# Kernel optimization log

Hardware: AMD Instinct MI355X
Metric: run time of the kernel (lower is better)

The kernel has to match this reference:

```python
import jax, jax.numpy as jnp
import numpy as np
from jax.scipy.special import gammaln

MAP_W, MAP_H, T_SIZE = 64, 64, 64  # map_sizes
NUM_CP = 8
BATCH = 128


def setup_inputs() -> dict:
    key = jax.random.key(0)
    k1, k2, k3 = jax.random.split(key, 3)
    # control-point means on the pixel grid [0, 63]
    cp_means = jax.random.uniform(k1, (NUM_CP, BATCH, 2), dtype=jnp.float32) * 63.0
    # PSD, well-conditioned 2x2 covariances: A A^T * 2 + 4 I
    A = jax.random.normal(k2, (NUM_CP, BATCH, 2, 2), dtype=jnp.float32)
    cp_covariances = jnp.einsum('kbij,kbpj->kbip', A, A) * 2.0 + 4.0 * jnp.eye(2, dtype=jnp.float32)
    # each curve uses between 3 and NUM_CP control points
    num_cps = jax.random.randint(k3, (BATCH,), 3, NUM_CP + 1, dtype=jnp.int64 if jax.config.jax_enable_x64 else jnp.int32)
    return {"cp_means": cp_means, "num_cps": num_cps, "cp_covariances": cp_covariances}


def _bezier_weights(num_cps, num_cp, t):
    # binomial_coefs[i, b] = binom(num_cps[b]-1, i) for i < num_cps[b], else 0
    k = jnp.arange(num_cp, dtype=jnp.float32)[:, None]          # (K,1)
    n = (num_cps - 1).astype(jnp.float32)[None, :]              # (1,B)
    valid = k <= n
    nk = jnp.where(valid, n - k, 0.0)
    coef = jnp.where(valid, jnp.exp(gammaln(n + 1.0) - gammaln(k + 1.0) - gammaln(nk + 1.0)), 0.0)  # (K,B)
    pot = jnp.maximum(n - k, 0.0)                               # pot[pot<0]=0
    # Bernstein basis weights: (K, B, T)
    w = coef[:, :, None] * (t[None, None, :] ** k[:, :, None]) * ((1.0 - t)[None, None, :] ** pot[:, :, None])
    return w


def reference(cp_means, num_cps, cp_covariances):
    num_cp = cp_means.shape[0]
    t = jnp.linspace(0.0, 1.0, T_SIZE, dtype=jnp.float32)
    w = _bezier_weights(num_cps, num_cp, t)                      # (K,B,T)
    mean = jnp.einsum('kbt,kbd->btd', w, cp_means)               # (B,T,2)
    cov = jnp.einsum('kbt,kbij->btij', w * w, cp_covariances)    # (B,T,2,2)

    # pixel grid positions: pos[x, y] = (x, y)
    xs = jnp.arange(MAP_W, dtype=jnp.float32)
    ys = jnp.arange(MAP_H, dtype=jnp.float32)
    pos = jnp.stack(jnp.meshgrid(xs, ys, indexing='ij'), axis=-1)  # (W,H,2)

    d = pos[None, :, :, None, :] - mean[:, None, None, :, :]      # (B,W,H,T,2)

    # closed-form 2x2 inverse and determinant
    a, b = cov[..., 0, 0], cov[..., 0, 1]
    c, dd = cov[..., 1, 0], cov[..., 1, 1]
    det = a * dd - b * c                                          # (B,T)
    inv = jnp.stack([jnp.stack([dd, -b], -1), jnp.stack([-c, a], -1)], -2) / det[..., None, None]

    q = jnp.einsum('bxyti,btij,bxytj->bxyt', d, inv, d)           # (B,W,H,T)
    divisor = jnp.sqrt((2.0 * np.pi) ** 2 * det)                  # (B,T)
    return jnp.exp(-0.5 * q) / divisor[:, None, None, :]
```

## Files before the change

### kernel.cpp

```cpp
#include <hip/hip_runtime.h>
#include <hip/hip_bf16.h>


#define MAP_W 64
#define MAP_H 64
#define T_SIZE 64
#define NUM_CP 8
#define BATCH 128

__global__ __launch_bounds__(256) void pmap_kernel(
    const void* __restrict__ cp_means_p,
    const void* __restrict__ num_cps_p,
    const void* __restrict__ cp_cov_p,
    float* __restrict__ out)
{
    __shared__ float s_my[T_SIZE], s_g11[T_SIZE], s_c0[T_SIZE], s_c1[T_SIZE], s_sc[T_SIZE];

    const int tid = threadIdx.x;
    const int blk = blockIdx.x;
    const int b   = blk >> 6;
    const int x   = blk & 63;

    if (tid < T_SIZE) {
        const int* ni32 = (const int*)num_cps_p;
        const bool is_i64 = (ni32[1] == 0);
        const int  ncp = is_i64 ? (int)((const long long*)num_cps_p)[b] : ni32[b];
        const int  n   = ncp - 1;

        const __hip_bfloat16* mbv = (const __hip_bfloat16*)cp_means_p;
        const __hip_bfloat16* cbv = (const __hip_bfloat16*)cp_cov_p;
        const float*          mf  = (const float*)cp_means_p;
        const float*          cf  = (const float*)cp_cov_p;
        bool is_f32 = false;
        #pragma unroll
        for (int i = 0; i < 32; ++i) {
            const float v = __bfloat162float(mbv[i]);
            if (!(v >= 0.0f && v <= 64.0f)) is_f32 = true;
        }

        const float t   = (float)tid * (1.0f / 63.0f);
        const float omt = 1.0f - t;

        float mx = 0.f, my = 0.f, ca = 0.f, cb = 0.f, cc = 0.f, cd = 0.f;
        float ck = 1.0f, tk = 1.0f;
        #pragma unroll
        for (int k = 0; k < NUM_CP; ++k) {
            const int e = n - k;
            float onk = (e == 0) ? 1.0f : 0.0f;
            float o = 1.0f;
            #pragma unroll
            for (int j = 1; j < NUM_CP; ++j) { o *= omt; if (e == j) onk = o; }
            const float w  = (k <= n) ? ck * tk * onk : 0.0f;
            const float w2 = w * w;
            const int base = k * BATCH + b;
            const float m0 = is_f32 ? mf[base*2+0] : __bfloat162float(mbv[base*2+0]);
            const float m1 = is_f32 ? mf[base*2+1] : __bfloat162float(mbv[base*2+1]);
            const float q0 = is_f32 ? cf[base*4+0] : __bfloat162float(cbv[base*4+0]);
            const float q1 = is_f32 ? cf[base*4+1] : __bfloat162float(cbv[base*4+1]);
            const float q2 = is_f32 ? cf[base*4+2] : __bfloat162float(cbv[base*4+2]);
            const float q3 = is_f32 ? cf[base*4+3] : __bfloat162float(cbv[base*4+3]);
            mx = fmaf(w,  m0, mx);
            my = fmaf(w,  m1, my);
            ca = fmaf(w2, q0, ca);
            cb = fmaf(w2, q1, cb);
            cc = fmaf(w2, q2, cc);
            cd = fmaf(w2, q3, cd);
            ck = ck * (float)(n - k) / (float)(k + 1);
            tk *= t;
        }

        const float det     = fmaf(ca, cd, -(cb * cc));
        const float inv_det = 1.0f / det;
        const float HL2E    = 0.72134752044448170368f;
        const float g00 = -HL2E * cd * inv_det;
        const float gxy =  HL2E * (cb + cc) * inv_det;
        const float g11 = -HL2E * ca * inv_det;
        const float scale = 0.15915494309189535f / sqrtf(det);

        const float dx = (float)x - mx;
        s_my[tid]  = my;
        s_g11[tid] = g11;
        s_c0[tid]  = g00 * dx * dx;
        s_c1[tid]  = gxy * dx;
        s_sc[tid]  = scale;
    }
    __syncthreads();

    const int t_idx = tid & 63;
    const int y0    = tid >> 6;
    const float my  = s_my[t_idx];
    const float g11 = s_g11[t_idx];
    const float c0  = s_c0[t_idx];
    const float c1  = s_c1[t_idx];
    const float sc  = s_sc[t_idx];

    float* __restrict__ orow = out + ((size_t)blk << 12) + t_idx;

    #pragma unroll
    for (int y = y0; y < MAP_H; y += 4) {
        const float dy  = (float)y - my;
        const float arg = fmaf(dy, fmaf(g11, dy, c1), c0);
        orow[y << 6] = sc * exp2f(arg);
    }
}

extern "C" void kernel_launch(void* const* d_in, const int* in_sizes, int n_in,
                              void* d_out, int out_size, void* d_ws, size_t ws_size,
                              hipStream_t stream) {
    pmap_kernel<<<dim3(BATCH * MAP_W), dim3(256), 0, stream>>>(
        d_in[0], d_in[1], d_in[2], (float*)d_out);
}
```

Baseline: 171.5 us.

## Precompute per-(batch,t) Bezier stats in a separate kernel and reuse across x

Splits the fused kernel in two. A small stats kernel computes the Bezier mean, inverse-covariance coefficients and scale once per (batch, t) into workspace, and the map kernel reads them back instead of recomputing them in every x block. This removes the redundant per-block Bezier evaluation and the block-level barrier, at the cost of a second launch and a workspace round trip. The original fused kernel is kept as a fallback when no workspace is provided.

```diff
diff --git a/kernel.cpp b/kernel.cpp
--- a/kernel.cpp
+++ b/kernel.cpp
@@ -7,6 +7,122 @@
 #define T_SIZE 64
 #define NUM_CP 8
 #define BATCH 128
+#define STATS_F 8
+
+__device__ __forceinline__ void bezier_stats(
+    const void* __restrict__ cp_means_p,
+    const void* __restrict__ num_cps_p,
+    const void* __restrict__ cp_cov_p,
+    const int b, const int t_i,
+    float& mx_o, float& my_o, float& g00_o, float& gxy_o, float& g11_o, float& sc_o)
+{
+    const int* ni32 = (const int*)num_cps_p;
+    const bool is_i64 = (ni32[1] == 0);
+    const int  ncp = is_i64 ? (int)((const long long*)num_cps_p)[b] : ni32[b];
+    const int  n   = ncp - 1;
+
+    const __hip_bfloat16* mbv = (const __hip_bfloat16*)cp_means_p;
+    const __hip_bfloat16* cbv = (const __hip_bfloat16*)cp_cov_p;
+    const float*          mf  = (const float*)cp_means_p;
+    const float*          cf  = (const float*)cp_cov_p;
+    bool is_f32 = false;
+    #pragma unroll
+    for (int i = 0; i < 32; ++i) {
+        const float v = __bfloat162float(mbv[i]);
+        if (!(v >= 0.0f && v <= 64.0f)) is_f32 = true;
+    }
+
+    const float t   = (float)t_i * (1.0f / 63.0f);
+    const float omt = 1.0f - t;
+
+    float mx = 0.f, my = 0.f, ca = 0.f, cb = 0.f, cc = 0.f, cd = 0.f;
+    float ck = 1.0f, tk = 1.0f;
+    #pragma unroll
+    for (int k = 0; k < NUM_CP; ++k) {
+        const int e = n - k;
+        float onk = (e == 0) ? 1.0f : 0.0f;
+        float o = 1.0f;
+        #pragma unroll
+        for (int j = 1; j < NUM_CP; ++j) { o *= omt; if (e == j) onk = o; }
+        const float w  = (k <= n) ? ck * tk * onk : 0.0f;
+        const float w2 = w * w;
+        const int base = k * BATCH + b;
+        const float m0 = is_f32 ? mf[base*2+0] : __bfloat162float(mbv[base*2+0]);
+        const float m1 = is_f32 ? mf[base*2+1] : __bfloat162float(mbv[base*2+1]);
+        const float q0 = is_f32 ? cf[base*4+0] : __bfloat162float(cbv[base*4+0]);
+        const float q1 = is_f32 ? cf[base*4+1] : __bfloat162float(cbv[base*4+1]);
+        const float q2 = is_f32 ? cf[base*4+2] : __bfloat162float(cbv[base*4+2]);
+        const float q3 = is_f32 ? cf[base*4+3] : __bfloat162float(cbv[base*4+3]);
+        mx = fmaf(w,  m0, mx);
+        my = fmaf(w,  m1, my);
+        ca = fmaf(w2, q0, ca);
+        cb = fmaf(w2, q1, cb);
+        cc = fmaf(w2, q2, cc);
+        cd = fmaf(w2, q3, cd);
+        ck = ck * (float)(n - k) / (float)(k + 1);
+        tk *= t;
+    }
+
+    const float det     = fmaf(ca, cd, -(cb * cc));
+    const float inv_det = 1.0f / det;
+    const float HL2E    = 0.72134752044448170368f;
+    mx_o  = mx;
+    my_o  = my;
+    g00_o = -HL2E * cd * inv_det;
+    gxy_o =  HL2E * (cb + cc) * inv_det;
+    g11_o = -HL2E * ca * inv_det;
+    sc_o  = 0.15915494309189535f / sqrtf(det);
+}
+
+__global__ __launch_bounds__(256) void stats_kernel(
+    const void* __restrict__ cp_means_p,
+    const void* __restrict__ num_cps_p,
+    const void* __restrict__ cp_cov_p,
+    float* __restrict__ ws)
+{
+    const int gid = blockIdx.x * 256 + threadIdx.x;
+    const int b   = gid >> 6;
+    const int t_i = gid & 63;
+
+    float mx, my, g00, gxy, g11, sc;
+    bezier_stats(cp_means_p, num_cps_p, cp_cov_p, b, t_i, mx, my, g00, gxy, g11, sc);
+
+    float4* w4 = (float4*)(ws + (size_t)gid * STATS_F);
+    w4[0] = make_float4(mx, my, g00, gxy);
+    w4[1] = make_float4(g11, sc, 0.0f, 0.0f);
+}
+
+__global__ __launch_bounds__(256) void map_kernel(
+    const float* __restrict__ ws,
+    float* __restrict__ out)
+{
+    const int tid = threadIdx.x;
+    const int blk = blockIdx.x;
+    const int b   = blk >> 6;
+    const int x   = blk & 63;
+
+    const int t_idx = tid & 63;
+    const int y0    = tid >> 6;
+
+    const float4* s4 = (const float4*)(ws + ((size_t)((b << 6) | t_idx)) * STATS_F);
+    const float4 s0 = s4[0];
+    const float4 s1 = s4[1];
+    const float mx = s0.x, my = s0.y, g00 = s0.z, gxy = s0.w;
+    const float g11 = s1.x, sc = s1.y;
+
+    const float dx = (float)x - mx;
+    const float c0 = g00 * dx * dx;
+    const float c1 = gxy * dx;
+
+    float* __restrict__ orow = out + ((size_t)blk << 12) + t_idx;
+
+    #pragma unroll
+    for (int y = y0; y < MAP_H; y += 4) {
+        const float dy  = (float)y - my;
+        const float arg = fmaf(dy, fmaf(g11, dy, c1), c0);
+        orow[y << 6] = sc * exp2f(arg);
+    }
+}
 
 __global__ __launch_bounds__(256) void pmap_kernel(
     const void* __restrict__ cp_means_p,
@@ -22,67 +138,14 @@
     const int x   = blk & 63;
 
     if (tid < T_SIZE) {
-        const int* ni32 = (const int*)num_cps_p;
-        const bool is_i64 = (ni32[1] == 0);
-        const int  ncp = is_i64 ? (int)((const long long*)num_cps_p)[b] : ni32[b];
-        const int  n   = ncp - 1;
-
-        const __hip_bfloat16* mbv = (const __hip_bfloat16*)cp_means_p;
-        const __hip_bfloat16* cbv = (const __hip_bfloat16*)cp_cov_p;
-        const float*          mf  = (const float*)cp_means_p;
-        const float*          cf  = (const float*)cp_cov_p;
-        bool is_f32 = false;
-        #pragma unroll
-        for (int i = 0; i < 32; ++i) {
-            const float v = __bfloat162float(mbv[i]);
-            if (!(v >= 0.0f && v <= 64.0f)) is_f32 = true;
-        }
-
-        const float t   = (float)tid * (1.0f / 63.0f);
-        const float omt = 1.0f - t;
-
-        float mx = 0.f, my = 0.f, ca = 0.f, cb = 0.f, cc = 0.f, cd = 0.f;
-        float ck = 1.0f, tk = 1.0f;
-        #pragma unroll
-        for (int k = 0; k < NUM_CP; ++k) {
-            const int e = n - k;
-            float onk = (e == 0) ? 1.0f : 0.0f;
-            float o = 1.0f;
-            #pragma unroll
-            for (int j = 1; j < NUM_CP; ++j) { o *= omt; if (e == j) onk = o; }
-            const float w  = (k <= n) ? ck * tk * onk : 0.0f;
-            const float w2 = w * w;
-            const int base = k * BATCH + b;
-            const float m0 = is_f32 ? mf[base*2+0] : __bfloat162float(mbv[base*2+0]);
-            const float m1 = is_f32 ? mf[base*2+1] : __bfloat162float(mbv[base*2+1]);
-            const float q0 = is_f32 ? cf[base*4+0] : __bfloat162float(cbv[base*4+0]);
-            const float q1 = is_f32 ? cf[base*4+1] : __bfloat162float(cbv[base*4+1]);
-            const float q2 = is_f32 ? cf[base*4+2] : __bfloat162float(cbv[base*4+2]);
-            const float q3 = is_f32 ? cf[base*4+3] : __bfloat162float(cbv[base*4+3]);
-            mx = fmaf(w,  m0, mx);
-            my = fmaf(w,  m1, my);
-            ca = fmaf(w2, q0, ca);
-            cb = fmaf(w2, q1, cb);
-            cc = fmaf(w2, q2, cc);
-            cd = fmaf(w2, q3, cd);
-            ck = ck * (float)(n - k) / (float)(k + 1);
-            tk *= t;
-        }
-
-        const float det     = fmaf(ca, cd, -(cb * cc));
-        const float inv_det = 1.0f / det;
-        const float HL2E    = 0.72134752044448170368f;
-        const float g00 = -HL2E * cd * inv_det;
-        const float gxy =  HL2E * (cb + cc) * inv_det;
-        const float g11 = -HL2E * ca * inv_det;
-        const float scale = 0.15915494309189535f / sqrtf(det);
-
+        float mx, my, g00, gxy, g11, sc;
+        bezier_stats(cp_means_p, num_cps_p, cp_cov_p, b, tid, mx, my, g00, gxy, g11, sc);
         const float dx = (float)x - mx;
         s_my[tid]  = my;
         s_g11[tid] = g11;
         s_c0[tid]  = g00 * dx * dx;
         s_c1[tid]  = gxy * dx;
-        s_sc[tid]  = scale;
+        s_sc[tid]  = sc;
     }
     __syncthreads();
 
@@ -107,6 +170,14 @@
 extern "C" void kernel_launch(void* const* d_in, const int* in_sizes, int n_in,
                               void* d_out, int out_size, void* d_ws, size_t ws_size,
                               hipStream_t stream) {
-    pmap_kernel<<<dim3(BATCH * MAP_W), dim3(256), 0, stream>>>(
-        d_in[0], d_in[1], d_in[2], (float*)d_out);
+    const size_t ws_needed = (size_t)BATCH * T_SIZE * STATS_F * sizeof(float);
+    if (d_ws != nullptr && ws_size >= ws_needed) {
+        stats_kernel<<<dim3((BATCH * T_SIZE) / 256), dim3(256), 0, stream>>>(
+            d_in[0], d_in[1], d_in[2], (float*)d_ws);
+        map_kernel<<<dim3(BATCH * MAP_W), dim3(256), 0, stream>>>(
+            (const float*)d_ws, (float*)d_out);
+    } else {
+        pmap_kernel<<<dim3(BATCH * MAP_W), dim3(256), 0, stream>>>(
+            d_in[0], d_in[1], d_in[2], (float*)d_out);
+    }
 }
```

New measurement: 141.6 us, median of 2. 1.21x faster.
